# Optimization experiments

Hardware: AMD Instinct MI355X
Metric: run time of the kernel (lower is better)

Reference implementation:

```python
import jax, jax.numpy as jnp
import numpy as np
import math

D_MODEL = 1024
DK = 64
N_HEADS = 16
B, S = 8, 1024


def setup_inputs() -> dict:
    key = jax.random.key(0)
    ks = jax.random.split(key, 9)
    scale_in = 1.0 / math.sqrt(D_MODEL)
    scale_cat = 1.0 / math.sqrt(N_HEADS * DK)
    x = jax.random.normal(ks[0], (B, S, D_MODEL), dtype=jnp.float32)
    # per-head stacked weights: [H, D, dk]
    Wq = jax.random.uniform(ks[1], (N_HEADS, D_MODEL, DK), jnp.float32, -scale_in, scale_in)
    bq = jax.random.uniform(ks[2], (N_HEADS, DK), jnp.float32, -scale_in, scale_in)
    Wk = jax.random.uniform(ks[3], (N_HEADS, D_MODEL, DK), jnp.float32, -scale_in, scale_in)
    bk = jax.random.uniform(ks[4], (N_HEADS, DK), jnp.float32, -scale_in, scale_in)
    Wv = jax.random.uniform(ks[5], (N_HEADS, D_MODEL, DK), jnp.float32, -scale_in, scale_in)
    bv = jax.random.uniform(ks[6], (N_HEADS, DK), jnp.float32, -scale_in, scale_in)
    Wo = jax.random.uniform(ks[7], (N_HEADS * DK, DK), jnp.float32, -scale_cat, scale_cat)
    bo = jax.random.uniform(ks[8], (DK,), jnp.float32, -scale_cat, scale_cat)
    return {"input_vector": x, "Wq": Wq, "bq": bq, "Wk": Wk, "bk": bk,
            "Wv": Wv, "bv": bv, "Wo": Wo, "bo": bo}


def reference(input_vector, Wq, bq, Wk, bk, Wv, bv, Wo, bo):
    # per-head linear projections + ReLU (heads batched via einsum)
    # q/k/v: [B, H, S, dk]
    q = jax.nn.relu(jnp.einsum('bsd,hdk->bhsk', input_vector, Wq) + bq[None, :, None, :])
    k = jax.nn.relu(jnp.einsum('bsd,hdk->bhsk', input_vector, Wk) + bk[None, :, None, :])
    v = jax.nn.relu(jnp.einsum('bsd,hdk->bhsk', input_vector, Wv) + bv[None, :, None, :])
    # raw attention scores (returned unscaled, like the torch module's `att`)
    att = jnp.einsum('bhqk,bhsk->bhqs', q, k)  # [B, H, S, S]
    probs = jax.nn.softmax(att / math.sqrt(DK), axis=-1)
    heads = jnp.einsum('bhqs,bhsk->bhqk', probs, v)  # [B, H, S, dk]
    # concat heads along feature dim: [B, S, H*dk]
    z = heads.transpose(0, 2, 1, 3).reshape(heads.shape[0], heads.shape[2], -1)
    z_out = jax.nn.relu(z @ Wo + bo)
    return (z_out, att)
```

## Files before the change

### kernel.cpp

```cpp
#include <hip/hip_runtime.h>


typedef __bf16 bf16x8 __attribute__((ext_vector_type(8)));
typedef float f32x4 __attribute__((ext_vector_type(4)));
typedef unsigned short u16x8 __attribute__((ext_vector_type(8)));
typedef unsigned short u16x4 __attribute__((ext_vector_type(4)));

typedef __attribute__((address_space(1))) unsigned int as1_u32;
typedef __attribute__((address_space(3))) unsigned int as3_u32;

#define MFMA16(a, b, c) __builtin_amdgcn_mfma_f32_16x16x32_bf16(a, b, c, 0, 0, 0)

__device__ __forceinline__ void gload_lds16(const void* g, void* l) {
  __builtin_amdgcn_global_load_lds((const as1_u32*)g, (as3_u32*)l, 16, 0, 0);
}

__device__ __forceinline__ unsigned short f2bf(float f) {
  union { float f; unsigned u; } a; a.f = f;
  unsigned r = a.u + 0x7FFFu + ((a.u >> 16) & 1u);
  return (unsigned short)(r >> 16);
}

__global__ __launch_bounds__(256) void pack_all(const float* __restrict__ x, const float* __restrict__ Wq,
                                                const float* __restrict__ Wk, const float* __restrict__ Wv,
                                                const float* __restrict__ Wo, const float* __restrict__ bq,
                                                const float* __restrict__ bk, const float* __restrict__ bv,
                                                ushort* __restrict__ xb, ushort* __restrict__ Wp,
                                                ushort* __restrict__ Wop, float* __restrict__ bqkv) {
  const int bid = blockIdx.x;
  if (bid < 8192) {
    const size_t i = ((size_t)bid * 256 + threadIdx.x) * 4;
    const float4 v = *(const float4*)(x + i);
    u16x4 o; o[0] = f2bf(v.x); o[1] = f2bf(v.y); o[2] = f2bf(v.z); o[3] = f2bf(v.w);
    *(u16x4*)(xb + i) = o;
  } else if (bid < 20480) {
    const int b2 = bid - 8192;
    const int swz = (b2 & 7) * 1536 + (b2 >> 3);
    const int o = swz * 256 + threadIdx.x;
    const int n = o >> 10, d = o & 1023;
    const int proj = n >> 10, hk = n & 1023;
    const float* W = proj == 0 ? Wq : (proj == 1 ? Wk : Wv);
    const int h = hk >> 6, kk = hk & 63;
    Wp[o] = f2bf(W[((size_t)h * 1024 + d) * 64 + kk]);
  } else {
    const int idx = (bid - 20480) * 256 + threadIdx.x;
    if (idx < 65536) {
      const int n = idx >> 10, c = idx & 1023;
      Wop[idx] = f2bf(Wo[c * 64 + n]);
    } else if (idx < 65536 + 3072) {
      const int n = idx - 65536;
      const int proj = n >> 10;
      const float* bb = proj == 0 ? bq : (proj == 1 ? bk : bv);
      bqkv[n] = bb[n & 1023];
    }
  }
}

__global__ __launch_bounds__(256) void gemm_qkv(const ushort* __restrict__ xb, const ushort* __restrict__ Wp,
                                                const float* __restrict__ bqkv, ushort* __restrict__ qo,
                                                ushort* __restrict__ ko, ushort* __restrict__ vTo) {
  __shared__ ushort As[128 * 32], Bs[128 * 32];
  const int bid = blockIdx.x;
  const int xcd = bid & 7, idx = bid >> 3;
  const int bx = idx >> 3, by = xcd * 8 + (idx & 7);
  const int t = threadIdx.x, w = t >> 6, l = t & 63, lg = l >> 4, lr = l & 15;
  const int m0 = by * 128, n0 = bx * 128;
  const int wm = w >> 1, wn = w & 1;
  const int srow = l >> 2, sslot = l & 3;
  f32x4 acc[4][4] = {};
  for (int kt = 0; kt < 32; ++kt) {
    __syncthreads();
#pragma unroll
    for (int c = 0; c < 2; ++c) {
      const int cc = w * 2 + c;
      const int row = cc * 16 + srow;
      gload_lds16(xb + (size_t)(m0 + row) * 1024 + kt * 32 + sslot * 8, &As[cc * 512]);
      gload_lds16(Wp + (size_t)(n0 + row) * 1024 + kt * 32 + sslot * 8, &Bs[cc * 512]);
    }
    __syncthreads();
    bf16x8 af[4], bfr[4];
#pragma unroll
    for (int mt = 0; mt < 4; ++mt)
      af[mt] = *(const bf16x8*)(&As[(wm * 64 + mt * 16 + lr) * 32 + lg * 8]);
#pragma unroll
    for (int nt = 0; nt < 4; ++nt)
      bfr[nt] = *(const bf16x8*)(&Bs[(wn * 64 + nt * 16 + lr) * 32 + lg * 8]);
#pragma unroll
    for (int mt = 0; mt < 4; ++mt)
#pragma unroll
      for (int nt = 0; nt < 4; ++nt)
        acc[mt][nt] = MFMA16(af[mt], bfr[nt], acc[mt][nt]);
  }
#pragma unroll
  for (int nt = 0; nt < 4; ++nt) {
    const int n = n0 + wn * 64 + nt * 16 + lr;
    const float bias = bqkv[n];
    const int proj = n >> 10, h = (n >> 6) & 15, dk = n & 63;
#pragma unroll
    for (int mt = 0; mt < 4; ++mt) {
      const int mb = m0 + wm * 64 + mt * 16 + lg * 4;
      const int b = mb >> 10, s = mb & 1023;
      float vv[4];
#pragma unroll
      for (int j = 0; j < 4; ++j) {
        float a = acc[mt][nt][j] + bias;
        vv[j] = a > 0.f ? a : 0.f;
      }
      if (proj == 2) {
        u16x4 o; o[0] = f2bf(vv[0]); o[1] = f2bf(vv[1]); o[2] = f2bf(vv[2]); o[3] = f2bf(vv[3]);
        *(u16x4*)(vTo + ((size_t)(b * 16 + h) * 64 + dk) * 1024 + s) = o;
      } else {
        ushort* op = proj == 0 ? qo : ko;
#pragma unroll
        for (int j = 0; j < 4; ++j)
          op[((size_t)(b * 16 + h) * 1024 + s + j) * 64 + dk] = f2bf(vv[j]);
      }
    }
  }
}

__global__ __launch_bounds__(256) void attn_kernel(const ushort* __restrict__ qg, const ushort* __restrict__ kg,
                                                   const ushort* __restrict__ vT, float* __restrict__ att,
                                                   ushort* __restrict__ heads) {
  const int bid = blockIdx.x;
  const int swz = (bid & 7) * 256 + (bid >> 3);
  const int qt = swz & 15, bh = swz >> 4;
  const int t = threadIdx.x, w = t >> 6, l = t & 63;
  const int lg = l >> 4, lr = l & 15;
  __shared__ ushort Ks[128 * 64];
  __shared__ ushort Vs[64 * 128];
  __shared__ ushort p_q[4][16][40];
  __shared__ float s_st[4][16][40];

  const ushort* qb = qg + (size_t)bh * 65536;
  const ushort* kb = kg + (size_t)bh * 65536;
  const ushort* vb = vT + (size_t)bh * 65536;
  const int qrow0 = qt * 64 + w * 16;

  const bf16x8 qf0 = *(const bf16x8*)(qb + (qrow0 + lr) * 64 + lg * 8);
  const bf16x8 qf1 = *(const bf16x8*)(qb + (qrow0 + lr) * 64 + 32 + lg * 8);

  const int krow = l >> 3, kch = l & 7;
  const int vrow = l >> 4, vch = l & 15;
  const int frow = l >> 3, fcol = (l & 7) * 4;

  const float C2 = 0.125f * 1.44269504f;
  f32x4 oacc[4] = {};
  float lsum = 0.f;
  float* attw = att + ((size_t)bh * 1024 + qrow0) * 1024;

  for (int g = 0; g < 8; ++g) {
    const int kv0 = g * 128;
    __syncthreads();
#pragma unroll
    for (int c2 = 0; c2 < 4; ++c2) {
      const int call = w * 4 + c2;
      const int r = call * 8 + krow;
      gload_lds16(kb + (size_t)(kv0 + r) * 64 + ((kch ^ (r & 7)) * 8), &Ks[call * 512]);
      const int rv = call * 4 + vrow;
      gload_lds16(vb + (size_t)rv * 1024 + kv0 + ((vch ^ (rv & 15)) * 8), &Vs[call * 512]);
    }
    __syncthreads();
    f32x4 sf[8];
#pragma unroll
    for (int f = 0; f < 8; ++f) {
      const int r = f * 16 + lr;
      const bf16x8 kf0 = *(const bf16x8*)(&Ks[r * 64 + ((lg ^ (r & 7)) * 8)]);
      const bf16x8 kf1 = *(const bf16x8*)(&Ks[r * 64 + (((4 + lg) ^ (r & 7)) * 8)]);
      f32x4 s = {};
      s = MFMA16(kf0, qf0, s);
      s = MFMA16(kf1, qf1, s);
      sf[f] = s;
    }
#pragma unroll
    for (int s = 0; s < 4; ++s) {
#pragma unroll
      for (int fi = 0; fi < 2; ++fi) {
        const int f = 2 * s + fi;
        u16x4 pk;
#pragma unroll
        for (int j = 0; j < 4; ++j) {
          const float p = exp2f(sf[f][j] * C2);
          lsum += p;
          pk[j] = f2bf(p);
        }
        *(u16x4*)(&p_q[w][lr][fi * 16 + lg * 4]) = pk;
        *(f32x4*)(&s_st[w][lr][fi * 16 + lg * 4]) = sf[f];
      }
      asm volatile("s_waitcnt lgkmcnt(0)" ::: "memory");
      __builtin_amdgcn_sched_barrier(0);
      const bf16x8 pa = *(const bf16x8*)(&p_q[w][lr][lg * 8]);
#pragma unroll
      for (int i = 0; i < 2; ++i) {
        const int r = i * 8 + frow;
        const f32x4 fv = *(const f32x4*)(&s_st[w][r][fcol]);
        __builtin_nontemporal_store(fv,
            (f32x4*)(attw + (size_t)r * 1024 + kv0 + s * 32 + fcol));
      }
#pragma unroll
      for (int nt = 0; nt < 4; ++nt) {
        const int r = nt * 16 + lr;
        const bf16x8 vf = *(const bf16x8*)(&Vs[r * 128 + (((s * 4 + lg) ^ lr) * 8)]);
        oacc[nt] = MFMA16(pa, vf, oacc[nt]);
      }
    }
  }
  lsum += __shfl_xor(lsum, 16, 64);
  lsum += __shfl_xor(lsum, 32, 64);
  float rdiv[4];
#pragma unroll
  for (int j = 0; j < 4; ++j) rdiv[j] = 1.f / __shfl(lsum, lg * 4 + j, 16);
  const int b = bh >> 4, h = bh & 15;
#pragma unroll
  for (int nt = 0; nt < 4; ++nt)
#pragma unroll
    for (int j = 0; j < 4; ++j)
      __builtin_nontemporal_store(f2bf(oacc[nt][j] * rdiv[j]),
          heads + (size_t)(b * 1024 + qrow0 + lg * 4 + j) * 1024 + h * 64 + nt * 16 + lr);
}

__global__ __launch_bounds__(256) void gemm_out(const ushort* __restrict__ z, const ushort* __restrict__ Wop,
                                                const float* __restrict__ bo, float* __restrict__ out) {
  __shared__ float red[2][16][64];
  const int t = threadIdx.x, w = t >> 6, l = t & 63, lg = l >> 4, lr = l & 15;
  const int wm = w & 1, kh = w >> 1;
  const int m0 = blockIdx.x * 32 + wm * 16;
  f32x4 acc[4] = {};
  for (int kk = kh * 16; kk < kh * 16 + 16; ++kk) {
    bf16x8 af = *(const bf16x8*)(z + (size_t)(m0 + lr) * 1024 + kk * 32 + lg * 8);
#pragma unroll
    for (int nt = 0; nt < 4; ++nt) {
      bf16x8 bfr = *(const bf16x8*)(Wop + (size_t)(nt * 16 + lr) * 1024 + kk * 32 + lg * 8);
      acc[nt] = MFMA16(af, bfr, acc[nt]);
    }
  }
  if (kh == 1) {
#pragma unroll
    for (int nt = 0; nt < 4; ++nt)
#pragma unroll
      for (int j = 0; j < 4; ++j) red[wm][lg * 4 + j][nt * 16 + lr] = acc[nt][j];
  }
  __syncthreads();
  if (kh == 0) {
#pragma unroll
    for (int nt = 0; nt < 4; ++nt) {
      const int n = nt * 16 + lr;
      const float bb = bo[n];
#pragma unroll
      for (int j = 0; j < 4; ++j) {
        const int m = m0 + lg * 4 + j;
        float vv = acc[nt][j] + red[wm][lg * 4 + j][n] + bb;
        out[(size_t)m * 64 + n] = vv > 0.f ? vv : 0.f;
      }
    }
  }
}

extern "C" void kernel_launch(void* const* d_in, const int* in_sizes, int n_in,
                              void* d_out, int out_size, void* d_ws, size_t ws_size,
                              hipStream_t stream) {
  const float* x  = (const float*)d_in[0];
  const float* Wq = (const float*)d_in[1];
  const float* bq = (const float*)d_in[2];
  const float* Wk = (const float*)d_in[3];
  const float* bk = (const float*)d_in[4];
  const float* Wv = (const float*)d_in[5];
  const float* bv = (const float*)d_in[6];
  const float* Wo = (const float*)d_in[7];
  const float* bo = (const float*)d_in[8];
  float* out = (float*)d_out;
  float* att = out + 524288;

  char* ws = (char*)d_ws;
  size_t off = 0;
  ushort* xb  = (ushort*)(ws + off); off += (size_t)8192 * 1024 * 2;
  ushort* Wp  = (ushort*)(ws + off); off += (size_t)3072 * 1024 * 2;
  ushort* Wop = (ushort*)(ws + off); off += (size_t)64 * 1024 * 2;
  float* bqkv = (float*)(ws + off);  off += (size_t)3072 * 4;
  ushort* q   = (ushort*)(ws + off); off += (size_t)128 * 1024 * 64 * 2;
  ushort* k   = (ushort*)(ws + off); off += (size_t)128 * 1024 * 64 * 2;
  ushort* vT  = (ushort*)(ws + off); off += (size_t)128 * 64 * 1024 * 2;
  ushort* hds = (ushort*)(ws + off); off += (size_t)8192 * 1024 * 2;
  (void)ws_size; (void)in_sizes; (void)n_in; (void)out_size;

  pack_all<<<dim3(20749), dim3(256), 0, stream>>>(x, Wq, Wk, Wv, Wo, bq, bk, bv,
                                                  xb, Wp, Wop, bqkv);
  gemm_qkv<<<dim3(1536), dim3(256), 0, stream>>>(xb, Wp, bqkv, q, k, vT);
  attn_kernel<<<dim3(2048), dim3(256), 0, stream>>>(q, k, vT, att, hds);
  gemm_out<<<dim3(256), dim3(256), 0, stream>>>(hds, Wop, bo, out);
}
```

Before: 228.3 us.

## Transpose QKV weights via LDS tiles and double K-step with swizzled LDS in GEMM

```diff
diff --git a/kernel.cpp b/kernel.cpp
--- a/kernel.cpp
+++ b/kernel.cpp
@@ -27,23 +27,38 @@
                                                 const float* __restrict__ bk, const float* __restrict__ bv,
                                                 ushort* __restrict__ xb, ushort* __restrict__ Wp,
                                                 ushort* __restrict__ Wop, float* __restrict__ bqkv) {
+  __shared__ float tile[64][65];
   const int bid = blockIdx.x;
   if (bid < 8192) {
     const size_t i = ((size_t)bid * 256 + threadIdx.x) * 4;
     const float4 v = *(const float4*)(x + i);
     u16x4 o; o[0] = f2bf(v.x); o[1] = f2bf(v.y); o[2] = f2bf(v.z); o[3] = f2bf(v.w);
     *(u16x4*)(xb + i) = o;
-  } else if (bid < 20480) {
-    const int b2 = bid - 8192;
-    const int swz = (b2 & 7) * 1536 + (b2 >> 3);
-    const int o = swz * 256 + threadIdx.x;
-    const int n = o >> 10, d = o & 1023;
-    const int proj = n >> 10, hk = n & 1023;
+  } else if (bid < 8960) {
+    const int b3 = bid - 8192;
+    const int proj = b3 >> 8, rem = b3 & 255;
+    const int h = rem >> 4, dt = rem & 15;
     const float* W = proj == 0 ? Wq : (proj == 1 ? Wk : Wv);
-    const int h = hk >> 6, kk = hk & 63;
-    Wp[o] = f2bf(W[((size_t)h * 1024 + d) * 64 + kk]);
+    const int r = threadIdx.x >> 2, cc = (threadIdx.x & 3) * 16;
+    const float* src = W + ((size_t)h * 1024 + dt * 64 + r) * 64 + cc;
+#pragma unroll
+    for (int i = 0; i < 4; ++i) {
+      const float4 v = *(const float4*)(src + i * 4);
+      tile[r][cc + i * 4 + 0] = v.x; tile[r][cc + i * 4 + 1] = v.y;
+      tile[r][cc + i * 4 + 2] = v.z; tile[r][cc + i * 4 + 3] = v.w;
+    }
+    __syncthreads();
+    const int kk = threadIdx.x >> 2, dc = (threadIdx.x & 3) * 16;
+    u16x8 o0, o1;
+#pragma unroll
+    for (int i = 0; i < 8; ++i) o0[i] = f2bf(tile[dc + i][kk]);
+#pragma unroll
+    for (int i = 0; i < 8; ++i) o1[i] = f2bf(tile[dc + 8 + i][kk]);
+    ushort* dst = Wp + (size_t)(proj * 1024 + h * 64 + kk) * 1024 + dt * 64 + dc;
+    *(u16x8*)dst = o0;
+    *(u16x8*)(dst + 8) = o1;
   } else {
-    const int idx = (bid - 20480) * 256 + threadIdx.x;
+    const int idx = (bid - 8960) * 256 + threadIdx.x;
     if (idx < 65536) {
       const int n = idx >> 10, c = idx & 1023;
       Wop[idx] = f2bf(Wo[c * 64 + n]);
@@ -59,37 +74,45 @@
 __global__ __launch_bounds__(256) void gemm_qkv(const ushort* __restrict__ xb, const ushort* __restrict__ Wp,
                                                 const float* __restrict__ bqkv, ushort* __restrict__ qo,
                                                 ushort* __restrict__ ko, ushort* __restrict__ vTo) {
-  __shared__ ushort As[128 * 32], Bs[128 * 32];
+  __shared__ ushort As[128 * 64], Bs[128 * 64];
   const int bid = blockIdx.x;
   const int xcd = bid & 7, idx = bid >> 3;
   const int bx = idx >> 3, by = xcd * 8 + (idx & 7);
   const int t = threadIdx.x, w = t >> 6, l = t & 63, lg = l >> 4, lr = l & 15;
   const int m0 = by * 128, n0 = bx * 128;
   const int wm = w >> 1, wn = w & 1;
-  const int srow = l >> 2, sslot = l & 3;
+  const int r8 = l >> 3, ch = l & 7;
   f32x4 acc[4][4] = {};
-  for (int kt = 0; kt < 32; ++kt) {
-    __syncthreads();
-#pragma unroll
-    for (int c = 0; c < 2; ++c) {
-      const int cc = w * 2 + c;
-      const int row = cc * 16 + srow;
-      gload_lds16(xb + (size_t)(m0 + row) * 1024 + kt * 32 + sslot * 8, &As[cc * 512]);
-      gload_lds16(Wp + (size_t)(n0 + row) * 1024 + kt * 32 + sslot * 8, &Bs[cc * 512]);
-    }
-    __syncthreads();
-    bf16x8 af[4], bfr[4];
-#pragma unroll
-    for (int mt = 0; mt < 4; ++mt)
-      af[mt] = *(const bf16x8*)(&As[(wm * 64 + mt * 16 + lr) * 32 + lg * 8]);
-#pragma unroll
-    for (int nt = 0; nt < 4; ++nt)
-      bfr[nt] = *(const bf16x8*)(&Bs[(wn * 64 + nt * 16 + lr) * 32 + lg * 8]);
-#pragma unroll
-    for (int mt = 0; mt < 4; ++mt)
-#pragma unroll
-      for (int nt = 0; nt < 4; ++nt)
-        acc[mt][nt] = MFMA16(af[mt], bfr[nt], acc[mt][nt]);
+  for (int kt = 0; kt < 16; ++kt) {
+    __syncthreads();
+#pragma unroll
+    for (int c2 = 0; c2 < 4; ++c2) {
+      const int c = w * 4 + c2;
+      const int row = c * 8 + r8;
+      const int sc = (ch ^ (row & 7)) * 8;
+      gload_lds16(xb + (size_t)(m0 + row) * 1024 + kt * 64 + sc, &As[c * 512]);
+      gload_lds16(Wp + (size_t)(n0 + row) * 1024 + kt * 64 + sc, &Bs[c * 512]);
+    }
+    __syncthreads();
+#pragma unroll
+    for (int hk = 0; hk < 2; ++hk) {
+      bf16x8 af[4], bfr[4];
+#pragma unroll
+      for (int mt = 0; mt < 4; ++mt) {
+        const int row = wm * 64 + mt * 16 + lr;
+        af[mt] = *(const bf16x8*)(&As[row * 64 + (((hk * 4 + lg) ^ (row & 7)) * 8)]);
+      }
+#pragma unroll
+      for (int nt = 0; nt < 4; ++nt) {
+        const int row = wn * 64 + nt * 16 + lr;
+        bfr[nt] = *(const bf16x8*)(&Bs[row * 64 + (((hk * 4 + lg) ^ (row & 7)) * 8)]);
+      }
+#pragma unroll
+      for (int mt = 0; mt < 4; ++mt)
+#pragma unroll
+        for (int nt = 0; nt < 4; ++nt)
+          acc[mt][nt] = MFMA16(af[mt], bfr[nt], acc[mt][nt]);
+    }
   }
 #pragma unroll
   for (int nt = 0; nt < 4; ++nt) {
@@ -283,8 +306,8 @@
   ushort* hds = (ushort*)(ws + off); off += (size_t)8192 * 1024 * 2;
   (void)ws_size; (void)in_sizes; (void)n_in; (void)out_size;
 
-  pack_all<<<dim3(20749), dim3(256), 0, stream>>>(x, Wq, Wk, Wv, Wo, bq, bk, bv,
-                                                  xb, Wp, Wop, bqkv);
+  pack_all<<<dim3(9229), dim3(256), 0, stream>>>(x, Wq, Wk, Wv, Wo, bq, bk, bv,
+                                                 xb, Wp, Wop, bqkv);
   gemm_qkv<<<dim3(1536), dim3(256), 0, stream>>>(xb, Wp, bqkv, q, k, vT);
   attn_kernel<<<dim3(2048), dim3(256), 0, stream>>>(q, k, vT, att, hds);
   gemm_out<<<dim3(256), dim3(256), 0, stream>>>(hds, Wop, bo, out);
```

Result: faster. 218.1 us (-4.4%).
